# Performance work log

Hardware: AMD Instinct MI355X
Metric: run time of the kernel (lower is better)

The kernel has to match this reference:

```python
import jax, jax.numpy as jnp
import numpy as np

EPS = 1e-6

def _rmsnorm(x, scale):
    # RMSNorm over last axis (TPNorm pre-norm)
    var = jnp.mean(jnp.square(x), axis=-1, keepdims=True)
    return x * jax.lax.rsqrt(var + EPS) * scale


def setup_inputs() -> dict:
    key = jax.random.key(0)
    ks = jax.random.split(key, 6)
    B, S, D, H, Dh = 2, 2048, 1024, 16, 64
    x = jax.random.normal(ks[0], (B, S, D), dtype=jnp.float32)
    norm_scale = jnp.ones((D,), dtype=jnp.float32)
    # lecun_normal-like scaling: std = 1/sqrt(fan_in)
    wq = jax.random.normal(ks[1], (D, H, Dh), dtype=jnp.float32) / np.sqrt(D)
    wk = jax.random.normal(ks[2], (D, H, Dh), dtype=jnp.float32) / np.sqrt(D)
    wv = jax.random.normal(ks[3], (D, H, Dh), dtype=jnp.float32) / np.sqrt(D)
    w_out = jax.random.normal(ks[4], (H, Dh, D), dtype=jnp.float32) / np.sqrt(H * Dh)
    b_out = jnp.zeros((D,), dtype=jnp.float32)
    return {"x": x, "norm_scale": norm_scale, "wq": wq, "wk": wk, "wv": wv,
            "w_out": w_out, "b_out": b_out}


def reference(x, norm_scale, wq, wk, wv, w_out, b_out):
    dtype = x.dtype
    softmax_dtype = jnp.float32
    h = _rmsnorm(x, norm_scale)                                  # [B,S,D]
    q = jnp.einsum('bsd,dhe->bshe', h, wq)                       # [B,S,H,Dh]
    k = jnp.einsum('bsd,dhe->bshe', h, wk)
    v = jnp.einsum('bsd,dhe->bshe', h, wv)
    head_dim = q.shape[-1]
    scale = head_dim ** (-0.5)
    q = (q * scale).astype(softmax_dtype)
    kf = k.astype(softmax_dtype)
    weights = jnp.einsum('bqhd,bkhd->bhqk', q, kf)               # [B,H,S,S] fp32
    weights = jax.nn.softmax(weights, axis=-1).astype(dtype)
    new_vals = jnp.einsum('bhqk,bkhd->bqhd', weights, v).astype(dtype)
    out = jnp.einsum('bqhe,hed->bqd', new_vals, w_out) + b_out   # [B,S,D]
    return out
```

## Files before the change

### kernel.cpp

```cpp
#include <hip/hip_runtime.h>

typedef unsigned short u16;
typedef unsigned int   u32;
typedef __attribute__((ext_vector_type(8))) short bf16x8;
typedef __attribute__((ext_vector_type(4))) float f32x4;

#define SEQ 2048
#define DIM 1024
#define NH  16
#define DH  64
#define NROW 4096

static __device__ __forceinline__ u16 f2bf(float f){
  u32 u; __builtin_memcpy(&u, &f, 4);
  u32 r = (u + 0x7fffu + ((u >> 16) & 1u)) >> 16;
  return (u16)r;
}
static __device__ __forceinline__ u32 pack2bf(float a, float b){
  u32 ua, ub; __builtin_memcpy(&ua, &a, 4); __builtin_memcpy(&ub, &b, 4);
  return ((ua + 0x8000u) >> 16) | ((ub + 0x8000u) & 0xFFFF0000u);
}
static __device__ __forceinline__ u32 cvt_pk_bf16(float a, float b){
  u32 r;
  asm("v_cvt_pk_bf16_f32 %0, %1, %2" : "=v"(r) : "v"(a), "v"(b));
  return r;
}

#define GLD_LDS(gp, lp) \
  __builtin_amdgcn_global_load_lds( \
      (const __attribute__((address_space(1))) void*)(gp), \
      (__attribute__((address_space(3))) void*)(lp), 16, 0, 0)

#define WAIT_VM(N) asm volatile("s_waitcnt vmcnt(" #N ")" ::: "memory")
#define CFENCE()   asm volatile("" ::: "memory")

__global__ __launch_bounds__(256) void k_rmsnorm(const float* __restrict__ x,
                                                 const float* __restrict__ sc,
                                                 u16* __restrict__ h){
  int row = blockIdx.x, t = threadIdx.x;
  float4 v = ((const float4*)(x + (size_t)row * DIM))[t];
  float ss = v.x*v.x + v.y*v.y + v.z*v.z + v.w*v.w;
  #pragma unroll
  for (int d = 32; d; d >>= 1) ss += __shfl_down(ss, d, 64);
  __shared__ float red[4];
  if ((t & 63) == 0) red[t >> 6] = ss;
  __syncthreads();
  float tot = red[0] + red[1] + red[2] + red[3];
  float rms = rsqrtf(tot * (1.0f / DIM) + 1e-6f);
  float4 s4 = ((const float4*)sc)[t];
  u16 ov[4];
  ov[0] = f2bf(v.x * rms * s4.x);
  ov[1] = f2bf(v.y * rms * s4.y);
  ov[2] = f2bf(v.z * rms * s4.z);
  ov[3] = f2bf(v.w * rms * s4.w);
  ((uint2*)(h + (size_t)row * DIM))[t] = *(uint2*)ov;
}

__global__ __launch_bounds__(256) void k_wtrans(const float* __restrict__ in0,
                                                const float* __restrict__ in1,
                                                const float* __restrict__ in2,
                                                u16* __restrict__ outT){
  __shared__ u16 tile[64][68];
  int t = threadIdx.x;
  int c0 = blockIdx.x * 64;
  int r0 = blockIdx.y * 64;
  int z = blockIdx.z;
  const float* in = (z == 0) ? in0 : ((z == 1) ? in1 : in2);
  u16* out = outT + (size_t)z * (1u << 20);
  #pragma unroll
  for (int i = 0; i < 4; i++){
    int idx = t + 256 * i;
    int r = idx >> 4, c4 = (idx & 15) * 4;
    float4 v = *(const float4*)&in[(size_t)(r0 + r) * 1024 + c0 + c4];
    u16 pk[4] = {f2bf(v.x), f2bf(v.y), f2bf(v.z), f2bf(v.w)};
    *(uint2*)&tile[r][c4] = *(uint2*)pk;
  }
  __syncthreads();
  #pragma unroll
  for (int i = 0; i < 2; i++){
    int c = t + 256 * i;
    int n = c >> 3, koff = (c & 7) * 8;
    alignas(16) u16 vals[8];
    #pragma unroll
    for (int j = 0; j < 8; j++) vals[j] = tile[koff + j][n];
    *(uint4*)&out[(size_t)(c0 + n) * 1024 + r0 + koff] = *(uint4*)vals;
  }
}

__global__ __launch_bounds__(256) void k_gemm(const u16* __restrict__ A,
                                              const u16* __restrict__ B0,
                                              const u16* __restrict__ B1,
                                              const u16* __restrict__ B2,
                                              void* __restrict__ C0,
                                              void* __restrict__ C1,
                                              void* __restrict__ C2,
                                              const float* __restrict__ bias,
                                              int qkv){
  __shared__ __align__(16) char smem[49152];
  u16 (*Al)[128][32] = (u16 (*)[128][32])smem;
  u16 (*Bl)[128][32] = (u16 (*)[128][32])(smem + 24576);
  int t = threadIdx.x, lane = t & 63, w = t >> 6;
  int wm = w & 1, wn = w >> 1;
  int mrow = lane & 15, quad = lane >> 4;

  int nwgs = qkv ? 768 : 256;
  int cpx = nwgs >> 3;
  int id = blockIdx.x;
  int wg = (id & 7) * cpx + (id >> 3);
  int z = wg >> 8;
  int rem = wg & 255;
  int m0 = (rem >> 3) << 7;
  int n0 = (rem & 7) << 7;
  const u16* Bt = (z == 0) ? B0 : ((z == 1) ? B1 : B2);

  int r0s = (t * 16) >> 6, off0 = ((t * 16) & 63) >> 1;
  int r1s = r0s + 64;

  const u16* Ap0 = &A [(size_t)(m0 + r0s) * 1024 + off0];
  const u16* Ap1 = &A [(size_t)(m0 + r1s) * 1024 + off0];
  const u16* Bp0 = &Bt[(size_t)(n0 + r0s) * 1024 + off0];
  const u16* Bp1 = &Bt[(size_t)(n0 + r1s) * 1024 + off0];

  f32x4 acc[4][4];
  #pragma unroll
  for (int ms = 0; ms < 4; ms++)
    #pragma unroll
    for (int ns = 0; ns < 4; ns++) acc[ms][ns] = (f32x4){0.f, 0.f, 0.f, 0.f};

  GLD_LDS(Ap0,      &Al[0][r0s][off0]);
  GLD_LDS(Ap1,      &Al[0][r1s][off0]);
  GLD_LDS(Bp0,      &Bl[0][r0s][off0]);
  GLD_LDS(Bp1,      &Bl[0][r1s][off0]);
  GLD_LDS(Ap0 + 32, &Al[1][r0s][off0]);
  GLD_LDS(Ap1 + 32, &Al[1][r1s][off0]);
  GLD_LDS(Bp0 + 32, &Bl[1][r0s][off0]);
  GLD_LDS(Bp1 + 32, &Bl[1][r1s][off0]);

  int cur = 0, pf = 2;
  for (int kt = 0; kt < 32; kt++){
    if (kt < 31) WAIT_VM(4); else WAIT_VM(0);
    __builtin_amdgcn_s_barrier();
    CFENCE();
    if (kt < 30){
      int K2 = (kt + 2) * 32;
      GLD_LDS(Ap0 + K2, &Al[pf][r0s][off0]);
      GLD_LDS(Ap1 + K2, &Al[pf][r1s][off0]);
      GLD_LDS(Bp0 + K2, &Bl[pf][r0s][off0]);
      GLD_LDS(Bp1 + K2, &Bl[pf][r1s][off0]);
    }
    bf16x8 af[4], bfr[4];
    #pragma unroll
    for (int ms = 0; ms < 4; ms++)
      af[ms] = *(const bf16x8*)&Al[cur][wm * 64 + ms * 16 + mrow][quad * 8];
    #pragma unroll
    for (int ns = 0; ns < 4; ns++)
      bfr[ns] = *(const bf16x8*)&Bl[cur][wn * 64 + ns * 16 + mrow][quad * 8];
    #pragma unroll
    for (int ms = 0; ms < 4; ms++)
      #pragma unroll
      for (int ns = 0; ns < 4; ns++)
        acc[ms][ns] = __builtin_amdgcn_mfma_f32_16x16x32_bf16(af[ms], bfr[ns], acc[ms][ns], 0, 0, 0);
    cur = (cur == 2) ? 0 : cur + 1;
    pf  = (pf  == 2) ? 0 : pf  + 1;
  }

  float qscale = (qkv && z == 0) ? 0.180336880111112f : 1.0f;

  __syncthreads();
  if (qkv && z == 2){
    #pragma unroll
    for (int ms = 0; ms < 4; ms++){
      #pragma unroll
      for (int ns = 0; ns < 4; ns++){
        int le = wn * 64 + ns * 16 + mrow;
        int ls = wm * 64 + ms * 16 + quad * 4;
        int ph = (ls >> 3) ^ (le & 7);
        uint2 pk = { pack2bf(acc[ms][ns][0], acc[ms][ns][1]),
                     pack2bf(acc[ms][ns][2], acc[ms][ns][3]) };
        *(uint2*)(smem + le * 256 + ph * 16 + (ls & 7) * 2) = pk;
      }
    }
    __syncthreads();
    int bidx = m0 >> 11, sl0 = m0 & 2047;
    u16* Cb = (u16*)C2;
    #pragma unroll
    for (int j = 0; j < 8; j++){
      int le = w * 32 + j * 4 + (lane >> 4);
      int c  = lane & 15;
      int ph = c ^ (le & 7);
      int hh2 = (n0 + le) >> 6, e = (n0 + le) & 63;
      uint4 v = *(uint4*)(smem + le * 256 + ph * 16);
      *(uint4*)&Cb[(size_t)((bidx * NH + hh2) * DH + e) * SEQ + sl0 + c * 8] = v;
    }
  } else if (qkv){
    #pragma unroll
    for (int ms = 0; ms < 4; ms++){
      #pragma unroll
      for (int ns = 0; ns < 4; ns++){
        int ld  = wn * 64 + ns * 16 + mrow;
        int lsb = wm * 64 + ms * 16 + quad * 4;
        #pragma unroll
        for (int r = 0; r < 4; r++){
          int ls = lsb + r;
          int ph = (ld >> 3) ^ (ls & 7);
          *(u16*)(smem + ls * 256 + ph * 16 + (ld & 7) * 2) = f2bf(acc[ms][ns][r] * qscale);
        }
      }
    }
    __syncthreads();
    u16* Cb = (u16*)((z == 0) ? C0 : C1);
    #pragma unroll
    for (int j = 0; j < 8; j++){
      int row = w * 32 + j * 4 + (lane >> 4);
      int c   = lane & 15;
      int ph  = c ^ (row & 7);
      uint4 v = *(uint4*)(smem + row * 256 + ph * 16);
      *(uint4*)&Cb[(size_t)(m0 + row) * 1024 + n0 + c * 8] = v;
    }
  } else {
    float* Cf = (float*)C0;
    for (int half = 0; half < 2; half++){
      if (wm == half){
        #pragma unroll
        for (int ms = 0; ms < 4; ms++){
          #pragma unroll
          for (int ns = 0; ns < 4; ns++){
            int ld  = wn * 64 + ns * 16 + mrow;
            int lsb = ms * 16 + quad * 4;
            #pragma unroll
            for (int r = 0; r < 4; r++){
              int ls = lsb + r;
              int ph = (ld >> 2) ^ (ls & 7);
              *(float*)(smem + ls * 512 + ph * 16 + (ld & 3) * 4) = acc[ms][ns][r];
            }
          }
        }
      }
      __syncthreads();
      #pragma unroll
      for (int j = 0; j < 8; j++){
        int row = w * 16 + j * 2 + (lane >> 5);
        int c   = lane & 31;
        int ph  = c ^ (row & 7);
        float4 v = *(float4*)(smem + row * 512 + ph * 16);
        float4 bb = *(const float4*)&bias[n0 + c * 4];
        v.x += bb.x; v.y += bb.y; v.z += bb.z; v.w += bb.w;
        *(float4*)&Cf[(size_t)(m0 + half * 64 + row) * 1024 + n0 + c * 4] = v;
      }
      __syncthreads();
    }
  }
}

__global__ __launch_bounds__(256) void k_attn(const u16* q,
                                              const u16* __restrict__ k,
                                              const u16* __restrict__ vt,
                                              u16* nv){
  __shared__ u16 Kl[3][64][64];
  __shared__ u16 Vl[3][64][64];
  int t = threadIdx.x, lane = t & 63, w = t >> 6;
  int mrow = lane & 15, quad = lane >> 4;
  int id = blockIdx.x;
  int wg = (id & 7) * 64 + (id >> 3);
  int s0 = (wg & 15) * 128;
  int bh = wg >> 4; int b = bh >> 4, hh = bh & 15;

  const u16* qrow0 = q + (size_t)((b * SEQ + s0 + w * 32 + mrow) * NH + hh) * DH;
  const u16* qrow1 = qrow0 + 16 * NH * DH;
  bf16x8 bq[2][2];
  bq[0][0] = *(const bf16x8*)(qrow0 + quad * 8);
  bq[0][1] = *(const bf16x8*)(qrow0 + 32 + quad * 8);
  bq[1][0] = *(const bf16x8*)(qrow1 + quad * 8);
  bq[1][1] = *(const bf16x8*)(qrow1 + 32 + quad * 8);

  int rw  = t >> 3;
  int fst = (rw & 3) | (((t >> 6) & 1) << 2);
  int lc  = (t & 7) ^ fst;
  const u16* kp = k  + ((size_t)b * SEQ + rw) * (NH * DH) + hh * DH + lc * 8;
  const u16* vp = vt + ((size_t)bh * DH + rw) * SEQ + lc * 8;

  int row0 = ((mrow >> 2) << 3) | (mrow & 3);
  int cK = (quad ^ ((mrow & 3) | (((mrow >> 2) & 1) << 2))) << 4;
  int cV = (quad ^ ((mrow & 3) | (((mrow >> 3) & 1) << 2))) << 4;

  f32x4 o[2][4];
  #pragma unroll
  for (int qg = 0; qg < 2; qg++)
    #pragma unroll
    for (int g = 0; g < 4; g++) o[qg][g] = (f32x4){0.f, 0.f, 0.f, 0.f};
  f32x4 accl[2];
  accl[0] = (f32x4){0.f, 0.f, 0.f, 0.f};
  accl[1] = (f32x4){0.f, 0.f, 0.f, 0.f};
  bf16x8 onesf;
  #pragma unroll
  for (int j = 0; j < 8; j++) onesf[j] = (short)0x3F80;

  #pragma unroll
  for (int pt = 0; pt < 2; pt++){
    u16* dK = (u16*)Kl[pt]; u16* dV = (u16*)Vl[pt];
    GLD_LDS(kp,                dK + (t << 3));
    GLD_LDS(kp + 32 * NH * DH, dK + 2048 + (t << 3));
    GLD_LDS(vp,                dV + (t << 3));
    GLD_LDS(vp + 32 * SEQ,     dV + 2048 + (t << 3));
    kp += 64 * NH * DH; vp += 64;
  }

  int cur = 0, pf = 2;
  for (int kt = 0; kt < 32; kt++){
    if (kt < 31) WAIT_VM(4); else WAIT_VM(0);
    __builtin_amdgcn_s_barrier();
    CFENCE();
    if (kt < 30){
      u16* dK = (u16*)Kl[pf]; u16* dV = (u16*)Vl[pf];
      GLD_LDS(kp,                dK + (t << 3));
      GLD_LDS(kp + 32 * NH * DH, dK + 2048 + (t << 3));
      GLD_LDS(vp,                dV + (t << 3));
      GLD_LDS(vp + 32 * SEQ,     dV + 2048 + (t << 3));
      kp += 64 * NH * DH; vp += 64;
    }

    const char* Kb = (const char*)Kl[cur];
    f32x4 sT[2][4];
    __builtin_amdgcn_s_setprio(1);
    #pragma unroll
    for (int g = 0; g < 4; g++){
      int rg = row0 + ((g & 1) << 2) + ((g >> 1) << 5);
      const char* rp = Kb + rg * 128;
      bf16x8 a0 = *(const bf16x8*)(rp + cK);
      bf16x8 a1 = *(const bf16x8*)(rp + (cK ^ 64));
      f32x4 z0 = (f32x4){0.f, 0.f, 0.f, 0.f};
      f32x4 z1 = (f32x4){0.f, 0.f, 0.f, 0.f};
      z0 = __builtin_amdgcn_mfma_f32_16x16x32_bf16(a0, bq[0][0], z0, 0, 0, 0);
      z1 = __builtin_amdgcn_mfma_f32_16x16x32_bf16(a0, bq[1][0], z1, 0, 0, 0);
      z0 = __builtin_amdgcn_mfma_f32_16x16x32_bf16(a1, bq[0][1], z0, 0, 0, 0);
      z1 = __builtin_amdgcn_mfma_f32_16x16x32_bf16(a1, bq[1][1], z1, 0, 0, 0);
      sT[0][g] = z0; sT[1][g] = z1;
    }
    __builtin_amdgcn_s_setprio(0);

    bf16x8 pb[2][2];
    #pragma unroll
    for (int qg = 0; qg < 2; qg++){
      u32 wd[8];
      #pragma unroll
      for (int g = 0; g < 4; g++){
        float e0 = __builtin_amdgcn_exp2f(sT[qg][g][0]);
        float e1 = __builtin_amdgcn_exp2f(sT[qg][g][1]);
        float e2 = __builtin_amdgcn_exp2f(sT[qg][g][2]);
        float e3 = __builtin_amdgcn_exp2f(sT[qg][g][3]);
        wd[g * 2]     = cvt_pk_bf16(e0, e1);
        wd[g * 2 + 1] = cvt_pk_bf16(e2, e3);
      }
      union { u32 u[4]; bf16x8 v; } U0, U1;
      U0.u[0] = wd[0]; U0.u[1] = wd[1]; U0.u[2] = wd[2]; U0.u[3] = wd[3];
      U1.u[0] = wd[4]; U1.u[1] = wd[5]; U1.u[2] = wd[6]; U1.u[3] = wd[7];
      pb[qg][0] = U0.v; pb[qg][1] = U1.v;
    }

    __builtin_amdgcn_s_setprio(1);
    #pragma unroll
    for (int qg = 0; qg < 2; qg++){
      accl[qg] = __builtin_amdgcn_mfma_f32_16x16x32_bf16(onesf, pb[qg][0], accl[qg], 0, 0, 0);
      accl[qg] = __builtin_amdgcn_mfma_f32_16x16x32_bf16(onesf, pb[qg][1], accl[qg], 0, 0, 0);
    }

    const char* Vb = (const char*)Vl[cur];
    #pragma unroll
    for (int ge = 0; ge < 4; ge++){
      const char* rp = Vb + (ge * 16 + mrow) * 128;
      bf16x8 v0 = *(const bf16x8*)(rp + cV);
      bf16x8 v1 = *(const bf16x8*)(rp + (cV ^ 64));
      o[0][ge] = __builtin_amdgcn_mfma_f32_16x16x32_bf16(v0, pb[0][0], o[0][ge], 0, 0, 0);
      o[1][ge] = __builtin_amdgcn_mfma_f32_16x16x32_bf16(v0, pb[1][0], o[1][ge], 0, 0, 0);
      o[0][ge] = __builtin_amdgcn_mfma_f32_16x16x32_bf16(v1, pb[0][1], o[0][ge], 0, 0, 0);
      o[1][ge] = __builtin_amdgcn_mfma_f32_16x16x32_bf16(v1, pb[1][1], o[1][ge], 0, 0, 0);
    }
    __builtin_amdgcn_s_setprio(0);

    cur = (cur == 2) ? 0 : cur + 1;
    pf  = (pf  == 2) ? 0 : pf  + 1;
  }

  float rl0 = 1.0f / accl[0][0];
  float rl1 = 1.0f / accl[1][0];
  u16* orow0 = nv + (size_t)((b * SEQ + s0 + w * 32 + mrow) * NH + hh) * DH;
  u16* orow1 = orow0 + 16 * NH * DH;
  #pragma unroll
  for (int ge = 0; ge < 4; ge++){
    uint2 pk0 = { cvt_pk_bf16(o[0][ge][0] * rl0, o[0][ge][1] * rl0),
                  cvt_pk_bf16(o[0][ge][2] * rl0, o[0][ge][3] * rl0) };
    *(uint2*)&orow0[ge * 16 + quad * 4] = pk0;
    uint2 pk1 = { cvt_pk_bf16(o[1][ge][0] * rl1, o[1][ge][1] * rl1),
                  cvt_pk_bf16(o[1][ge][2] * rl1, o[1][ge][3] * rl1) };
    *(uint2*)&orow1[ge * 16 + quad * 4] = pk1;
  }
}

extern "C" void kernel_launch(void* const* d_in, const int* in_sizes, int n_in,
                              void* d_out, int out_size, void* d_ws, size_t ws_size,
                              hipStream_t stream){
  const float* x   = (const float*)d_in[0];
  const float* nsc = (const float*)d_in[1];
  const float* wq  = (const float*)d_in[2];
  const float* wk  = (const float*)d_in[3];
  const float* wv  = (const float*)d_in[4];
  const float* wo  = (const float*)d_in[5];
  const float* bo  = (const float*)d_in[6];
  char* ws = (char*)d_ws;
  const size_t MB = (size_t)1 << 20;

  u16* qb  = (u16*)(ws);
  u16* kb  = (u16*)(ws + 8  * MB);
  u16* vtb = (u16*)(ws + 16 * MB);
  u16* h   = (u16*)d_out;
  u16* wT  = (u16*)((char*)d_out + 8 * MB);
  u16* wqT = wT;
  u16* wkT = wT + (1u << 20);
  u16* wvT = wT + (2u << 20);
  u16* woT = kb;

  k_rmsnorm<<<NROW, 256, 0, stream>>>(x, nsc, h);
  k_wtrans<<<dim3(16, 16, 3), 256, 0, stream>>>(wq, wk, wv, wT);
  k_gemm<<<dim3(768), 256, 0, stream>>>(h, wqT, wkT, wvT, qb, kb, vtb, nullptr, 1);
  k_attn<<<dim3(512), 256, 0, stream>>>(qb, kb, vtb, qb);
  k_wtrans<<<dim3(16, 16, 1), 256, 0, stream>>>(wo, wo, wo, woT);
  k_gemm<<<dim3(256), 256, 0, stream>>>(qb, woT, woT, woT, d_out, d_out, d_out, bo, 0);
}
```

Before: 192.8 us.

## Software-pipeline QK^T in attention and add dedicated 128x64 output-projection GEMM

The attention loop moves to a 4-deep K/V LDS ring and computes the next tile's QK^T scores ahead of the current tile's exp and PV MFMAs, so score MFMAs overlap with exp and V work. The output projection gets its own kernel with 128x64 tiles and 512 workgroups instead of 256, to fill more CUs, and a single-pass fp32 epilogue. The cost is more registers for the prefetched scores and more LDS in attention, which may lower occupancy.

```diff
diff --git a/kernel.cpp b/kernel.cpp
--- a/kernel.cpp
+++ b/kernel.cpp
@@ -93,9 +93,7 @@
                                               const u16* __restrict__ B2,
                                               void* __restrict__ C0,
                                               void* __restrict__ C1,
-                                              void* __restrict__ C2,
-                                              const float* __restrict__ bias,
-                                              int qkv){
+                                              void* __restrict__ C2){
   __shared__ __align__(16) char smem[49152];
   u16 (*Al)[128][32] = (u16 (*)[128][32])smem;
   u16 (*Bl)[128][32] = (u16 (*)[128][32])(smem + 24576);
@@ -103,10 +101,8 @@
   int wm = w & 1, wn = w >> 1;
   int mrow = lane & 15, quad = lane >> 4;
 
-  int nwgs = qkv ? 768 : 256;
-  int cpx = nwgs >> 3;
   int id = blockIdx.x;
-  int wg = (id & 7) * cpx + (id >> 3);
+  int wg = (id & 7) * 96 + (id >> 3);
   int z = wg >> 8;
   int rem = wg & 255;
   int m0 = (rem >> 3) << 7;
@@ -164,10 +160,10 @@
     pf  = (pf  == 2) ? 0 : pf  + 1;
   }
 
-  float qscale = (qkv && z == 0) ? 0.180336880111112f : 1.0f;
+  float qscale = (z == 0) ? 0.180336880111112f : 1.0f;
 
   __syncthreads();
-  if (qkv && z == 2){
+  if (z == 2){
     #pragma unroll
     for (int ms = 0; ms < 4; ms++){
       #pragma unroll
@@ -192,7 +188,7 @@
       uint4 v = *(uint4*)(smem + le * 256 + ph * 16);
       *(uint4*)&Cb[(size_t)((bidx * NH + hh2) * DH + e) * SEQ + sl0 + c * 8] = v;
     }
-  } else if (qkv){
+  } else {
     #pragma unroll
     for (int ms = 0; ms < 4; ms++){
       #pragma unroll
@@ -217,38 +213,98 @@
       uint4 v = *(uint4*)(smem + row * 256 + ph * 16);
       *(uint4*)&Cb[(size_t)(m0 + row) * 1024 + n0 + c * 8] = v;
     }
-  } else {
-    float* Cf = (float*)C0;
-    for (int half = 0; half < 2; half++){
-      if (wm == half){
-        #pragma unroll
-        for (int ms = 0; ms < 4; ms++){
-          #pragma unroll
-          for (int ns = 0; ns < 4; ns++){
-            int ld  = wn * 64 + ns * 16 + mrow;
-            int lsb = ms * 16 + quad * 4;
-            #pragma unroll
-            for (int r = 0; r < 4; r++){
-              int ls = lsb + r;
-              int ph = (ld >> 2) ^ (ls & 7);
-              *(float*)(smem + ls * 512 + ph * 16 + (ld & 3) * 4) = acc[ms][ns][r];
-            }
-          }
-        }
+  }
+}
+
+__global__ __launch_bounds__(256) void k_gemm_out(const u16* __restrict__ A,
+                                                  const u16* __restrict__ Bt,
+                                                  float* __restrict__ C,
+                                                  const float* __restrict__ bias){
+  __shared__ __align__(16) char smem[36864];
+  u16 (*Al)[128][32] = (u16 (*)[128][32])smem;
+  u16 (*Bl)[ 64][32] = (u16 (*)[ 64][32])(smem + 24576);
+  int t = threadIdx.x, lane = t & 63, w = t >> 6;
+  int wm = w & 1, wn = w >> 1;
+  int mrow = lane & 15, quad = lane >> 4;
+
+  int id = blockIdx.x;
+  int wg = (id & 7) * 64 + (id >> 3);
+  int m0 = (wg >> 4) << 7;
+  int n0 = (wg & 15) << 6;
+
+  int r0s = (t * 16) >> 6, off0 = ((t * 16) & 63) >> 1;
+  int r1s = r0s + 64;
+  int rB  = t >> 2, offB = (t & 3) * 8;
+
+  const u16* Ap0 = &A [(size_t)(m0 + r0s) * 1024 + off0];
+  const u16* Ap1 = &A [(size_t)(m0 + r1s) * 1024 + off0];
+  const u16* Bp  = &Bt[(size_t)(n0 + rB ) * 1024 + offB];
+
+  f32x4 acc[4][2];
+  #pragma unroll
+  for (int ms = 0; ms < 4; ms++)
+    #pragma unroll
+    for (int ns = 0; ns < 2; ns++) acc[ms][ns] = (f32x4){0.f, 0.f, 0.f, 0.f};
+
+  GLD_LDS(Ap0,      &Al[0][r0s][off0]);
+  GLD_LDS(Ap1,      &Al[0][r1s][off0]);
+  GLD_LDS(Bp,       &Bl[0][rB ][offB]);
+  GLD_LDS(Ap0 + 32, &Al[1][r0s][off0]);
+  GLD_LDS(Ap1 + 32, &Al[1][r1s][off0]);
+  GLD_LDS(Bp  + 32, &Bl[1][rB ][offB]);
+
+  int cur = 0, pf = 2;
+  for (int kt = 0; kt < 32; kt++){
+    if (kt < 31) WAIT_VM(3); else WAIT_VM(0);
+    __builtin_amdgcn_s_barrier();
+    CFENCE();
+    if (kt < 30){
+      int K2 = (kt + 2) * 32;
+      GLD_LDS(Ap0 + K2, &Al[pf][r0s][off0]);
+      GLD_LDS(Ap1 + K2, &Al[pf][r1s][off0]);
+      GLD_LDS(Bp  + K2, &Bl[pf][rB ][offB]);
+    }
+    bf16x8 af[4], bfr[2];
+    #pragma unroll
+    for (int ms = 0; ms < 4; ms++)
+      af[ms] = *(const bf16x8*)&Al[cur][wm * 64 + ms * 16 + mrow][quad * 8];
+    #pragma unroll
+    for (int ns = 0; ns < 2; ns++)
+      bfr[ns] = *(const bf16x8*)&Bl[cur][wn * 32 + ns * 16 + mrow][quad * 8];
+    #pragma unroll
+    for (int ms = 0; ms < 4; ms++)
+      #pragma unroll
+      for (int ns = 0; ns < 2; ns++)
+        acc[ms][ns] = __builtin_amdgcn_mfma_f32_16x16x32_bf16(af[ms], bfr[ns], acc[ms][ns], 0, 0, 0);
+    cur = (cur == 2) ? 0 : cur + 1;
+    pf  = (pf  == 2) ? 0 : pf  + 1;
+  }
+
+  __syncthreads();
+  #pragma unroll
+  for (int ms = 0; ms < 4; ms++){
+    #pragma unroll
+    for (int ns = 0; ns < 2; ns++){
+      int ld  = wn * 32 + ns * 16 + mrow;
+      int lsb = wm * 64 + ms * 16 + quad * 4;
+      #pragma unroll
+      for (int r = 0; r < 4; r++){
+        int ls = lsb + r;
+        int ph = (ld >> 2) ^ (ls & 15);
+        *(float*)(smem + ls * 256 + ph * 16 + (ld & 3) * 4) = acc[ms][ns][r];
       }
-      __syncthreads();
-      #pragma unroll
-      for (int j = 0; j < 8; j++){
-        int row = w * 16 + j * 2 + (lane >> 5);
-        int c   = lane & 31;
-        int ph  = c ^ (row & 7);
-        float4 v = *(float4*)(smem + row * 512 + ph * 16);
-        float4 bb = *(const float4*)&bias[n0 + c * 4];
-        v.x += bb.x; v.y += bb.y; v.z += bb.z; v.w += bb.w;
-        *(float4*)&Cf[(size_t)(m0 + half * 64 + row) * 1024 + n0 + c * 4] = v;
-      }
-      __syncthreads();
-    }
+    }
+  }
+  __syncthreads();
+  #pragma unroll
+  for (int j = 0; j < 8; j++){
+    int row = w * 32 + j * 4 + (lane >> 4);
+    int c   = lane & 15;
+    int ph  = c ^ (row & 15);
+    float4 v = *(float4*)(smem + row * 256 + ph * 16);
+    float4 bb = *(const float4*)&bias[n0 + c * 4];
+    v.x += bb.x; v.y += bb.y; v.z += bb.z; v.w += bb.w;
+    *(float4*)&C[(size_t)(m0 + row) * 1024 + n0 + c * 4] = v;
   }
 }
 
@@ -256,8 +312,8 @@
                                               const u16* __restrict__ k,
                                               const u16* __restrict__ vt,
                                               u16* nv){
-  __shared__ u16 Kl[3][64][64];
-  __shared__ u16 Vl[3][64][64];
+  __shared__ u16 Kl[4][64][64];
+  __shared__ u16 Vl[4][64][64];
   int t = threadIdx.x, lane = t & 63, w = t >> 6;
   int mrow = lane & 15, quad = lane >> 4;
   int id = blockIdx.x;
@@ -295,48 +351,59 @@
   #pragma unroll
   for (int j = 0; j < 8; j++) onesf[j] = (short)0x3F80;
 
-  #pragma unroll
-  for (int pt = 0; pt < 2; pt++){
-    u16* dK = (u16*)Kl[pt]; u16* dV = (u16*)Vl[pt];
-    GLD_LDS(kp,                dK + (t << 3));
-    GLD_LDS(kp + 32 * NH * DH, dK + 2048 + (t << 3));
-    GLD_LDS(vp,                dV + (t << 3));
-    GLD_LDS(vp + 32 * SEQ,     dV + 2048 + (t << 3));
-    kp += 64 * NH * DH; vp += 64;
-  }
-
-  int cur = 0, pf = 2;
+#define STAGE_KV(BUF) do{ \
+    u16* dK = (u16*)Kl[BUF]; u16* dV = (u16*)Vl[BUF]; \
+    GLD_LDS(kp,                dK + (t << 3)); \
+    GLD_LDS(kp + 32 * NH * DH, dK + 2048 + (t << 3)); \
+    GLD_LDS(vp,                dV + (t << 3)); \
+    GLD_LDS(vp + 32 * SEQ,     dV + 2048 + (t << 3)); \
+    kp += 64 * NH * DH; vp += 64; \
+  }while(0)
+
+#define QKT4(KB, S0, S1) do{ \
+    const char* Kb_ = (const char*)(KB); \
+    _Pragma("unroll") \
+    for (int g = 0; g < 4; g++){ \
+      int rg = row0 + ((g & 1) << 2) + ((g >> 1) << 5); \
+      const char* rp = Kb_ + rg * 128; \
+      bf16x8 a0 = *(const bf16x8*)(rp + cK); \
+      bf16x8 a1 = *(const bf16x8*)(rp + (cK ^ 64)); \
+      f32x4 z0 = (f32x4){0.f, 0.f, 0.f, 0.f}; \
+      f32x4 z1 = (f32x4){0.f, 0.f, 0.f, 0.f}; \
+      z0 = __builtin_amdgcn_mfma_f32_16x16x32_bf16(a0, bq[0][0], z0, 0, 0, 0); \
+      z1 = __builtin_amdgcn_mfma_f32_16x16x32_bf16(a0, bq[1][0], z1, 0, 0, 0); \
+      z0 = __builtin_amdgcn_mfma_f32_16x16x32_bf16(a1, bq[0][1], z0, 0, 0, 0); \
+      z1 = __builtin_amdgcn_mfma_f32_16x16x32_bf16(a1, bq[1][1], z1, 0, 0, 0); \
+      (S0)[g] = z0; (S1)[g] = z1; \
+    } \
+  }while(0)
+
+  STAGE_KV(0);
+  STAGE_KV(1);
+  STAGE_KV(2);
+  WAIT_VM(8);
+  __builtin_amdgcn_s_barrier();
+  CFENCE();
+
+  f32x4 sc0[4], sc1[4], sn0[4], sn1[4];
+  __builtin_amdgcn_s_setprio(1);
+  QKT4(Kl[0], sc0, sc1);
+  __builtin_amdgcn_s_setprio(0);
+
   for (int kt = 0; kt < 32; kt++){
-    if (kt < 31) WAIT_VM(4); else WAIT_VM(0);
+    int cb = kt & 3;
+    if (kt < 31){
+      if (kt < 30) WAIT_VM(4); else WAIT_VM(0);
+    }
     __builtin_amdgcn_s_barrier();
     CFENCE();
-    if (kt < 30){
-      u16* dK = (u16*)Kl[pf]; u16* dV = (u16*)Vl[pf];
-      GLD_LDS(kp,                dK + (t << 3));
-      GLD_LDS(kp + 32 * NH * DH, dK + 2048 + (t << 3));
-      GLD_LDS(vp,                dV + (t << 3));
-      GLD_LDS(vp + 32 * SEQ,     dV + 2048 + (t << 3));
-      kp += 64 * NH * DH; vp += 64;
-    }
-
-    const char* Kb = (const char*)Kl[cur];
-    f32x4 sT[2][4];
-    __builtin_amdgcn_s_setprio(1);
-    #pragma unroll
-    for (int g = 0; g < 4; g++){
-      int rg = row0 + ((g & 1) << 2) + ((g >> 1) << 5);
-      const char* rp = Kb + rg * 128;
-      bf16x8 a0 = *(const bf16x8*)(rp + cK);
-      bf16x8 a1 = *(const bf16x8*)(rp + (cK ^ 64));
-      f32x4 z0 = (f32x4){0.f, 0.f, 0.f, 0.f};
-      f32x4 z1 = (f32x4){0.f, 0.f, 0.f, 0.f};
-      z0 = __builtin_amdgcn_mfma_f32_16x16x32_bf16(a0, bq[0][0], z0, 0, 0, 0);
-      z1 = __builtin_amdgcn_mfma_f32_16x16x32_bf16(a0, bq[1][0], z1, 0, 0, 0);
-      z0 = __builtin_amdgcn_mfma_f32_16x16x32_bf16(a1, bq[0][1], z0, 0, 0, 0);
-      z1 = __builtin_amdgcn_mfma_f32_16x16x32_bf16(a1, bq[1][1], z1, 0, 0, 0);
-      sT[0][g] = z0; sT[1][g] = z1;
-    }
-    __builtin_amdgcn_s_setprio(0);
+    if (kt <= 28) STAGE_KV((kt + 3) & 3);
+
+    if (kt < 31){
+      __builtin_amdgcn_s_setprio(1);
+      QKT4(Kl[(kt + 1) & 3], sn0, sn1);
+      __builtin_amdgcn_s_setprio(0);
+    }
 
     bf16x8 pb[2][2];
     #pragma unroll
@@ -344,10 +411,11 @@
       u32 wd[8];
       #pragma unroll
       for (int g = 0; g < 4; g++){
-        float e0 = __builtin_amdgcn_exp2f(sT[qg][g][0]);
-        float e1 = __builtin_amdgcn_exp2f(sT[qg][g][1]);
-        float e2 = __builtin_amdgcn_exp2f(sT[qg][g][2]);
-        float e3 = __builtin_amdgcn_exp2f(sT[qg][g][3]);
+        f32x4 sg = qg ? sc1[g] : sc0[g];
+        float e0 = __builtin_amdgcn_exp2f(sg[0]);
+        float e1 = __builtin_amdgcn_exp2f(sg[1]);
+        float e2 = __builtin_amdgcn_exp2f(sg[2]);
+        float e3 = __builtin_amdgcn_exp2f(sg[3]);
         wd[g * 2]     = cvt_pk_bf16(e0, e1);
         wd[g * 2 + 1] = cvt_pk_bf16(e2, e3);
       }
@@ -363,8 +431,7 @@
       accl[qg] = __builtin_amdgcn_mfma_f32_16x16x32_bf16(onesf, pb[qg][0], accl[qg], 0, 0, 0);
       accl[qg] = __builtin_amdgcn_mfma_f32_16x16x32_bf16(onesf, pb[qg][1], accl[qg], 0, 0, 0);
     }
-
-    const char* Vb = (const char*)Vl[cur];
+    const char* Vb = (const char*)Vl[cb];
     #pragma unroll
     for (int ge = 0; ge < 4; ge++){
       const char* rp = Vb + (ge * 16 + mrow) * 128;
@@ -377,8 +444,10 @@
     }
     __builtin_amdgcn_s_setprio(0);
 
-    cur = (cur == 2) ? 0 : cur + 1;
-    pf  = (pf  == 2) ? 0 : pf  + 1;
+    if (kt < 31){
+      #pragma unroll
+      for (int g = 0; g < 4; g++){ sc0[g] = sn0[g]; sc1[g] = sn1[g]; }
+    }
   }
 
   float rl0 = 1.0f / accl[0][0];
@@ -394,6 +463,8 @@
                   cvt_pk_bf16(o[1][ge][2] * rl1, o[1][ge][3] * rl1) };
     *(uint2*)&orow1[ge * 16 + quad * 4] = pk1;
   }
+#undef STAGE_KV
+#undef QKT4
 }
 
 extern "C" void kernel_launch(void* const* d_in, const int* in_sizes, int n_in,
@@ -421,8 +492,8 @@
 
   k_rmsnorm<<<NROW, 256, 0, stream>>>(x, nsc, h);
   k_wtrans<<<dim3(16, 16, 3), 256, 0, stream>>>(wq, wk, wv, wT);
-  k_gemm<<<dim3(768), 256, 0, stream>>>(h, wqT, wkT, wvT, qb, kb, vtb, nullptr, 1);
+  k_gemm<<<dim3(768), 256, 0, stream>>>(h, wqT, wkT, wvT, qb, kb, vtb);
   k_attn<<<dim3(512), 256, 0, stream>>>(qb, kb, vtb, qb);
   k_wtrans<<<dim3(16, 16, 1), 256, 0, stream>>>(wo, wo, wo, woT);
-  k_gemm<<<dim3(256), 256, 0, stream>>>(qb, woT, woT, woT, d_out, d_out, d_out, bo, 0);
-}
+  k_gemm_out<<<dim3(512), 256, 0, stream>>>(qb, woT, (float*)d_out, bo);
+}
```

After: 186.2 us. 1.04x faster.
